# Kernel optimization log

Hardware: AMD Instinct MI355X
Metric: run time of the kernel (lower is better)

The kernel has to match this reference:

```python
import jax, jax.numpy as jnp
import numpy as np

B, T, NT, H, L, F, NH, R = 2, 1024, 30, 1024, 8, 2816, 16, 16
HD = H // NH
LORA_SCALE = 32.0 / 16.0  # lora_alpha / r
CLAMP = 10.0
EPS = 1e-6


def _rms(x, w):
    return x * jax.lax.rsqrt(jnp.mean(x * x, axis=-1, keepdims=True) + EPS) * w


def _rope(x):
    # x: [B,T,NH,HD] -- LLaMA rotary embedding
    half = HD // 2
    inv_freq = 1.0 / (10000.0 ** (jnp.arange(0, half, dtype=jnp.float32) / half))
    ang = jnp.arange(x.shape[1], dtype=jnp.float32)[:, None] * inv_freq  # [T,half]
    cos = jnp.concatenate([jnp.cos(ang), jnp.cos(ang)], -1)[None, :, None, :]
    sin = jnp.concatenate([jnp.sin(ang), jnp.sin(ang)], -1)[None, :, None, :]
    x1, x2 = x[..., :half], x[..., half:]
    return x * cos + jnp.concatenate([-x2, x1], -1) * sin


def _lora(x, W, A, Bm):
    # W: [in,out], A: [r,in], Bm: [out,r]  (dequantized base + LoRA update)
    return x @ W + ((x @ A.T) @ Bm.T) * LORA_SCALE


def setup_inputs():
    key = jax.random.key(0)
    ks = jax.random.split(key, 16)
    n = lambda k, s, sc=0.02: jax.random.normal(k, s, jnp.float32) * sc
    return {
        'x': jax.random.normal(ks[0], (B, T, NT), jnp.float32),
        'temperature': jnp.float32(1.0),
        'state_W': n(ks[1], (NT, H), 0.1),
        'state_b': jnp.zeros((H,), jnp.float32),
        'ln1': jnp.ones((L, H), jnp.float32),
        'ln2': jnp.ones((L, H), jnp.float32),
        'Wqkv': n(ks[2], (L, 3, H, H)),
        'Aqkv': n(ks[3], (L, 3, R, H)),
        'Bqkv': n(ks[4], (L, 3, H, R)),
        'Wo': n(ks[5], (L, H, H)),
        'Ao': n(ks[6], (L, R, H)),
        'Bo': n(ks[7], (L, H, R)),
        'Wgu': n(ks[8], (L, 2, H, F)),
        'Agu': n(ks[9], (L, 2, R, H)),
        'Bgu': n(ks[10], (L, 2, F, R)),
        'Wd': n(ks[11], (L, F, H)),
        'Ad': n(ks[12], (L, R, F)),
        'Bd': n(ks[13], (L, H, R)),
        'ln_f': jnp.ones((H,), jnp.float32),
        'head_W': n(ks[14], (H, NT + 1), 0.01),
        'head_b': jnp.zeros((NT + 1,), jnp.float32),
    }


def reference(x, temperature, state_W, state_b, ln1, ln2, Wqkv, Aqkv, Bqkv,
              Wo, Ao, Bo, Wgu, Agu, Bgu, Wd, Ad, Bd, ln_f, head_W, head_b):
    causal = jnp.tril(jnp.ones((T, T), bool))

    def layer(h, p):
        l1, l2, wqkv, aqkv, bqkv, wo, ao, bo, wgu, agu, bgu, wd, ad, bd = p
        hn = _rms(h, l1)
        qkv = jnp.einsum('bth,khd->kbtd', hn, wqkv)
        qkv = qkv + jnp.einsum('kbtr,kdr->kbtd',
                               jnp.einsum('bth,krh->kbtr', hn, aqkv), bqkv) * LORA_SCALE
        q = _rope(qkv[0].reshape(B, T, NH, HD))
        k = _rope(qkv[1].reshape(B, T, NH, HD))
        v = qkv[2].reshape(B, T, NH, HD)
        scores = jnp.einsum('bqhd,bkhd->bhqk', q, k) / np.sqrt(HD).astype(np.float32)
        scores = jnp.where(causal, scores, jnp.float32(-1e9))
        probs = jax.nn.softmax(scores, axis=-1)
        att = jnp.einsum('bhqk,bkhd->bqhd', probs, v).reshape(B, T, H)
        h = h + _lora(att, wo, ao, bo)
        hn2 = _rms(h, l2)
        gu = jnp.einsum('bth,khf->kbtf', hn2, wgu)
        gu = gu + jnp.einsum('kbtr,kfr->kbtf',
                             jnp.einsum('bth,krh->kbtr', hn2, agu), bgu) * LORA_SCALE
        act = jax.nn.silu(gu[0]) * gu[1]
        h = h + _lora(act, wd, ad, bd)
        return h, None

    h = x @ state_W + state_b  # state encoder -> inputs_embeds
    h, _ = jax.lax.scan(layer, h, (ln1, ln2, Wqkv, Aqkv, Bqkv, Wo, Ao, Bo,
                                   Wgu, Agu, Bgu, Wd, Ad, Bd))
    latent = _rms(h, ln_f)  # last hidden state
    logits = latent @ head_W + head_b
    logits_clamped = jnp.clip(logits, -CLAMP, CLAMP)
    portfolio_weights = jax.nn.softmax(logits_clamped / temperature, axis=-1)
    return portfolio_weights, logits_clamped
```

## Files before the change

### kernel.cpp

```cpp
#include <hip/hip_runtime.h>
#include <hip/hip_bf16.h>
#include <cstdint>

#define B_    2
#define T_    1024
#define NT_   30
#define H_    1024
#define L_    8
#define F_    2816
#define NH_   16
#define R_    16
#define HD_   64
#define M_    2048
#define NTP1_ 31

typedef unsigned short u16;
typedef short  s16x8 __attribute__((ext_vector_type(8)));
typedef unsigned short u16x4 __attribute__((ext_vector_type(4)));
typedef unsigned short u16x8 __attribute__((ext_vector_type(8)));
typedef float  f32x4 __attribute__((ext_vector_type(4)));

__device__ __forceinline__ u16 f2bf(float f){
  __hip_bfloat16 h = __float2bfloat16(f);
  return __builtin_bit_cast(unsigned short, h);
}
__device__ __forceinline__ float bf2f(u16 u){
  uint32_t v = (uint32_t)u << 16;
  return __builtin_bit_cast(float, v);
}

__device__ __forceinline__ void async16(const void* g, void* l){
  __builtin_amdgcn_global_load_lds((const __attribute__((address_space(1))) void*)g,
                                   (__attribute__((address_space(3))) void*)l, 16, 0, 0);
}

__global__ __launch_bounds__(256, 3) void fold_kernel(
    const float* __restrict__ W, const float* __restrict__ A,
    const float* __restrict__ Bm, u16* __restrict__ Wt,
    int K, int N, long strW, long strA, long strB, long strWt)
{
  const int mat = blockIdx.z;
  W  += (long)mat * strW;  A  += (long)mat * strA;
  Bm += (long)mat * strB;  Wt += (long)mat * strWt;
  const int k0 = blockIdx.x * 64, n0 = blockIdx.y * 64;
  __shared__ float Wt_s[64][65];
  __shared__ float As[16][64];
  __shared__ float Bs[64][20];
  const int tid = threadIdx.x;
  {
    const int kr = tid >> 4;
    const int n4 = (tid & 15) * 4;
    #pragma unroll
    for (int p = 0; p < 4; p++){
      int krow = p * 16 + kr;
      float4 w = *(const float4*)(W + (long)(k0 + krow) * N + n0 + n4);
      Wt_s[n4+0][krow] = w.x; Wt_s[n4+1][krow] = w.y;
      Wt_s[n4+2][krow] = w.z; Wt_s[n4+3][krow] = w.w;
    }
    const int r = tid >> 4, kc = (tid & 15) * 4;
    *(float4*)&As[r][kc] = *(const float4*)(A + (long)r * K + k0 + kc);
    const int nb = tid >> 2, r4 = (tid & 3) * 4;
    float4 b = *(const float4*)(Bm + (long)(n0 + nb) * 16 + r4);
    Bs[nb][r4+0]=b.x; Bs[nb][r4+1]=b.y; Bs[nb][r4+2]=b.z; Bs[nb][r4+3]=b.w;
  }
  __syncthreads();
  const int ko = (tid & 7) * 8;
  const int na = tid >> 3;
  float bq0[16], bq1[16];
  #pragma unroll
  for (int c = 0; c < 4; c++){
    *(float4*)&bq0[c*4] = *(const float4*)&Bs[na][c*4];
    *(float4*)&bq1[c*4] = *(const float4*)&Bs[na+32][c*4];
  }
  float l0[8] = {}, l1[8] = {};
  #pragma unroll
  for (int r = 0; r < 16; r++){
    float a[8];
    *(float4*)&a[0] = *(const float4*)&As[r][ko];
    *(float4*)&a[4] = *(const float4*)&As[r][ko+4];
    #pragma unroll
    for (int j = 0; j < 8; j++){
      l0[j] += a[j] * bq0[r];
      l1[j] += a[j] * bq1[r];
    }
  }
  u16x8 o0, o1;
  #pragma unroll
  for (int j = 0; j < 8; j++){
    o0[j] = f2bf(Wt_s[na][ko+j]    + 2.0f * l0[j]);
    o1[j] = f2bf(Wt_s[na+32][ko+j] + 2.0f * l1[j]);
  }
  *(u16x8*)(Wt + (long)(n0+na)*K    + k0 + ko) = o0;
  *(u16x8*)(Wt + (long)(n0+na+32)*K + k0 + ko) = o1;
}

__global__ __launch_bounds__(256) void embed_kernel(
    const float* __restrict__ x, const float* __restrict__ sw,
    const float* __restrict__ sb, float* __restrict__ h)
{
  const int m = blockIdx.x;
  const float* xr = x + (long)m * NT_;
  for (int jj = threadIdx.x; jj < H_; jj += 256){
    float acc = sb[jj];
    #pragma unroll
    for (int i = 0; i < NT_; i++) acc += xr[i] * sw[i * H_ + jj];
    h[(long)m * H_ + jj] = acc;
  }
}

__global__ __launch_bounds__(256) void rms_kernel(
    float* __restrict__ hsrc, const float* __restrict__ p0, const float* __restrict__ p1,
    const float* __restrict__ w, u16* __restrict__ outp, int fuse)
{
  const int m = blockIdx.x, t = threadIdx.x;
  float4 v = ((const float4*)(hsrc + (long)m * H_))[t];
  if (fuse){
    const float4 a = ((const float4*)(p0 + (long)m * H_))[t];
    const float4 b = ((const float4*)(p1 + (long)m * H_))[t];
    v.x += a.x + b.x; v.y += a.y + b.y; v.z += a.z + b.z; v.w += a.w + b.w;
    ((float4*)(hsrc + (long)m * H_))[t] = v;
  }
  float ss = v.x*v.x + v.y*v.y + v.z*v.z + v.w*v.w;
  #pragma unroll
  for (int off = 32; off >= 1; off >>= 1) ss += __shfl_xor(ss, off);
  __shared__ float red[4];
  if ((t & 63) == 0) red[t >> 6] = ss;
  __syncthreads();
  const float scale = rsqrtf((red[0]+red[1]+red[2]+red[3]) * (1.0f/H_) + 1e-6f);
  const float4 wv = ((const float4*)w)[t];
  u16x4 o;
  o[0] = f2bf(v.x*scale*wv.x); o[1] = f2bf(v.y*scale*wv.y);
  o[2] = f2bf(v.z*scale*wv.z); o[3] = f2bf(v.w*scale*wv.w);
  *(u16x4*)(outp + (long)m * H_ + t * 4) = o;
}

template<int OUTBF>
__global__ __launch_bounds__(256, 2) void gemm_bt(
    const u16* __restrict__ Ag, const u16* __restrict__ Btg, void* __restrict__ Cptr,
    int Ndim, int Klen, int Kstride, long zsA, long zsB, long zsC)
{
  Ag  += (long)blockIdx.z * zsA;
  Btg += (long)blockIdx.z * zsB;
  const int m0 = blockIdx.x * 128, n0 = blockIdx.y * 128;
  __shared__ alignas(16) u16 As[128 * 64];
  __shared__ alignas(16) u16 Bs[128 * 64];
  const int tid = threadIdx.x;
  const int wave = tid >> 6, lane = tid & 63;
  const int wm = (wave & 1) * 64, wn = (wave >> 1) * 64;
  const int fr = lane & 15, quad = lane >> 4;

  f32x4 acc[4][4] = {};

  for (int kt = 0; kt < Klen; kt += 64){
    __syncthreads();
    #pragma unroll
    for (int c = 0; c < 4; c++){
      int lin = c * 256 + tid;
      int row = lin >> 3, p = lin & 7;
      int gc = ((p ^ (row & 7)) * 8);
      async16(Ag  + (long)(m0 + row) * Kstride + kt + gc, As + lin * 8);
      async16(Btg + (long)(n0 + row) * Kstride + kt + gc, Bs + lin * 8);
    }
    __syncthreads();
    #pragma unroll
    for (int kk = 0; kk < 2; kk++){
      s16x8 af[4], bg[4];
      #pragma unroll
      for (int i = 0; i < 4; i++){
        int rA = wm + i * 16 + fr;
        af[i] = *(const s16x8*)(As + rA * 64 + (((kk*4 + quad) ^ (rA & 7)) * 8));
        int rB = wn + i * 16 + fr;
        bg[i] = *(const s16x8*)(Bs + rB * 64 + (((kk*4 + quad) ^ (rB & 7)) * 8));
      }
      #pragma unroll
      for (int i = 0; i < 4; i++)
        #pragma unroll
        for (int j = 0; j < 4; j++)
          acc[i][j] = __builtin_amdgcn_mfma_f32_16x16x32_bf16(af[i], bg[j], acc[i][j], 0, 0, 0);
    }
  }
  #pragma unroll
  for (int i = 0; i < 4; i++){
    int row0 = m0 + wm + i * 16 + quad * 4;
    #pragma unroll
    for (int j = 0; j < 4; j++){
      int col = n0 + wn + j * 16 + fr;
      #pragma unroll
      for (int r = 0; r < 4; r++){
        long idx = (long)(row0 + r) * Ndim + col;
        if (OUTBF){
          u16* C = (u16*)Cptr + (long)blockIdx.z * zsC;
          C[idx] = f2bf(acc[i][j][r]);
        } else {
          float* C = (float*)Cptr + (long)blockIdx.z * zsC;
          C[idx] = acc[i][j][r];
        }
      }
    }
  }
}

__global__ __launch_bounds__(256, 2) void gemm_gu(
    const u16* __restrict__ Ag, const u16* __restrict__ Bgw,
    const u16* __restrict__ Buw, u16* __restrict__ actb)
{
  const int m0 = blockIdx.x * 128, n0 = blockIdx.y * 128;
  __shared__ alignas(16) u16 As[128 * 64];
  __shared__ alignas(16) u16 Bg_[128 * 64];
  __shared__ alignas(16) u16 Bu_[128 * 64];
  const int tid = threadIdx.x;
  const int wave = tid >> 6, lane = tid & 63;
  const int wm = (wave & 1) * 64, wn = (wave >> 1) * 64;
  const int fr = lane & 15, quad = lane >> 4;

  f32x4 accg[4][4] = {}, accu[4][4] = {};

  for (int kt = 0; kt < H_; kt += 64){
    __syncthreads();
    #pragma unroll
    for (int c = 0; c < 4; c++){
      int lin = c * 256 + tid;
      int row = lin >> 3, p = lin & 7;
      int gc = ((p ^ (row & 7)) * 8);
      async16(Ag  + (long)(m0 + row) * H_ + kt + gc, As  + lin * 8);
      async16(Bgw + (long)(n0 + row) * H_ + kt + gc, Bg_ + lin * 8);
      async16(Buw + (long)(n0 + row) * H_ + kt + gc, Bu_ + lin * 8);
    }
    __syncthreads();
    #pragma unroll
    for (int kk = 0; kk < 2; kk++){
      s16x8 af[4], bb[4];
      #pragma unroll
      for (int i = 0; i < 4; i++){
        int rA = wm + i * 16 + fr;
        af[i] = *(const s16x8*)(As + rA * 64 + (((kk*4 + quad) ^ (rA & 7)) * 8));
      }
      #pragma unroll
      for (int i = 0; i < 4; i++){
        int rB = wn + i * 16 + fr;
        bb[i] = *(const s16x8*)(Bg_ + rB * 64 + (((kk*4 + quad) ^ (rB & 7)) * 8));
      }
      #pragma unroll
      for (int i = 0; i < 4; i++)
        #pragma unroll
        for (int j = 0; j < 4; j++)
          accg[i][j] = __builtin_amdgcn_mfma_f32_16x16x32_bf16(af[i], bb[j], accg[i][j], 0, 0, 0);
      #pragma unroll
      for (int i = 0; i < 4; i++){
        int rB = wn + i * 16 + fr;
        bb[i] = *(const s16x8*)(Bu_ + rB * 64 + (((kk*4 + quad) ^ (rB & 7)) * 8));
      }
      #pragma unroll
      for (int i = 0; i < 4; i++)
        #pragma unroll
        for (int j = 0; j < 4; j++)
          accu[i][j] = __builtin_amdgcn_mfma_f32_16x16x32_bf16(af[i], bb[j], accu[i][j], 0, 0, 0);
    }
  }
  #pragma unroll
  for (int i = 0; i < 4; i++){
    int row0 = m0 + wm + i * 16 + quad * 4;
    #pragma unroll
    for (int j = 0; j < 4; j++){
      int col = n0 + wn + j * 16 + fr;
      #pragma unroll
      for (int r = 0; r < 4; r++){
        float g = accg[i][j][r], u = accu[i][j][r];
        float act = g / (1.0f + __expf(-g)) * u;
        actb[(long)(row0 + r) * F_ + col] = f2bf(act);
      }
    }
  }
}

__global__ __launch_bounds__(256) void rope_vt_kernel(
    const u16* __restrict__ qkv, u16* __restrict__ qr, u16* __restrict__ kr,
    u16* __restrict__ vt)
{
  const int bid = blockIdx.x;
  if (bid < M_){
    const int m = bid;
    const int b = m >> 10, t = m & 1023;
    for (int w = threadIdx.x; w < 1024; w += 256){
      const int sel = w >> 9;
      const int hh  = (w >> 5) & 15;
      const int i   = w & 31;
      const u16* src = qkv + (long)m * 3072 + sel * 1024 + hh * HD_;
      float x1 = bf2f(src[i]), x2 = bf2f(src[i + 32]);
      float freq = exp2f((float)i * (-13.287712379549449f / 32.0f));
      float ang = (float)t * freq;
      float sn, cs; __sincosf(ang, &sn, &cs);
      u16* dst = (sel ? kr : qr) + ((long)((b * NH_ + hh) * T_ + t)) * HD_;
      dst[i]      = f2bf(x1 * cs - x2 * sn);
      dst[i + 32] = f2bf(x2 * cs + x1 * sn);
    }
  } else {
    const int v = bid - M_;
    const int bh = v >> 5, tch = v & 31;
    const int b = bh >> 4, hh = bh & 15;
    const int d = threadIdx.x & 63, tc = threadIdx.x >> 6;
    const int t0 = tch * 32 + tc * 8;
    const u16* src = qkv + (long)(b * T_ + t0) * 3072 + 2048 + hh * HD_ + d;
    u16x8 o;
    #pragma unroll
    for (int j = 0; j < 8; j++) o[j] = src[(long)j * 3072];
    *(u16x8*)(vt + ((long)bh * HD_ + d) * T_ + t0) = o;
  }
}

__global__ __launch_bounds__(256, 2) void attn_kernel(
    const u16* __restrict__ qr, const u16* __restrict__ kr,
    const u16* __restrict__ vt, u16* __restrict__ att)
{
  const int bh = blockIdx.y;
  const int b = bh >> 4, hh = bh & 15;
  __shared__ alignas(16) u16 Qs[64 * 64];
  __shared__ alignas(16) u16 Ks[128 * 64];
  __shared__ alignas(16) u16 Vs[64 * 128];
  __shared__ alignas(16) u16 Ps[64 * 136];
  const int tid = threadIdx.x;
  const int wave = tid >> 6, lane = tid & 63, fr = lane & 15, quad = lane >> 4;
  const int wrow = wave * 16;
  const u16* kgb = kr + (long)bh * T_ * HD_;
  const u16* vgb = vt + (long)bh * HD_ * T_;

  for (int pass = 0; pass < 2; pass++){
    const int qt = pass ? (15 - (int)blockIdx.x) : (int)blockIdx.x;
    __syncthreads();
    const u16* qg = qr + ((long)bh * T_ + qt * 64) * HD_;
    #pragma unroll
    for (int c = 0; c < 2; c++){
      int lin = c * 256 + tid, row = lin >> 3, p = lin & 7;
      async16(qg + row * HD_ + ((p ^ (row & 7)) * 8), Qs + lin * 8);
    }
    f32x4 o_acc[4] = {};
    float m_r[4] = {-1e30f, -1e30f, -1e30f, -1e30f};
    float l_r[4] = {};
    const int kmax = (qt * 64 + 63) >> 7;

    for (int kt = 0; kt <= kmax; kt++){
      __syncthreads();
      const u16* kg = kgb + (long)kt * 128 * HD_;
      #pragma unroll
      for (int c = 0; c < 4; c++){
        int lin = c * 256 + tid, row = lin >> 3, p = lin & 7;
        async16(kg + row * HD_ + ((p ^ (row & 7)) * 8), Ks + lin * 8);
      }
      #pragma unroll
      for (int c = 0; c < 4; c++){
        int lin = c * 256 + tid, row = lin >> 4, p = lin & 15;
        async16(vgb + (long)row * T_ + kt * 128 + ((p ^ (row & 15)) * 8), Vs + lin * 8);
      }
      __syncthreads();

      f32x4 s[8] = {};
      s16x8 aq[2];
      {
        int rA = wrow + fr;
        #pragma unroll
        for (int kk = 0; kk < 2; kk++)
          aq[kk] = *(const s16x8*)(Qs + rA * 64 + (((kk*4 + quad) ^ (rA & 7)) * 8));
      }
      #pragma unroll
      for (int ik = 0; ik < 8; ik++){
        #pragma unroll
        for (int kk = 0; kk < 2; kk++){
          int rB = ik * 16 + fr;
          s16x8 bk = *(const s16x8*)(Ks + rB * 64 + (((kk*4 + quad) ^ (rB & 7)) * 8));
          s[ik] = __builtin_amdgcn_mfma_f32_16x16x32_bf16(aq[kk], bk, s[ik], 0, 0, 0);
        }
      }
      const bool diag = (kt == kmax);
      #pragma unroll
      for (int r = 0; r < 4; r++){
        const int qgi = qt * 64 + wrow + quad * 4 + r;
        float tmax = -1e30f;
        #pragma unroll
        for (int ik = 0; ik < 8; ik++){
          float v = s[ik][r] * 0.125f;
          if (diag && (kt * 128 + ik * 16 + fr) > qgi) v = -1e9f;
          s[ik][r] = v;
          tmax = fmaxf(tmax, v);
        }
        #pragma unroll
        for (int off = 8; off >= 1; off >>= 1) tmax = fmaxf(tmax, __shfl_xor(tmax, off));
        const float mnew = fmaxf(m_r[r], tmax);
        const float alpha = __expf(m_r[r] - mnew);
        m_r[r] = mnew;
        float ts = 0.0f;
        const int prow = wrow + quad * 4 + r;
        #pragma unroll
        for (int ik = 0; ik < 8; ik++){
          float p = __expf(s[ik][r] - mnew);
          ts += p;
          Ps[prow * 136 + ik * 16 + fr] = f2bf(p);
        }
        #pragma unroll
        for (int off = 8; off >= 1; off >>= 1) ts += __shfl_xor(ts, off);
        l_r[r] = l_r[r] * alpha + ts;
        #pragma unroll
        for (int jd = 0; jd < 4; jd++) o_acc[jd][r] *= alpha;
      }
      #pragma unroll
      for (int kk2 = 0; kk2 < 4; kk2++){
        s16x8 ap = *(const s16x8*)(Ps + (wrow + fr) * 136 + kk2 * 32 + quad * 8);
        #pragma unroll
        for (int jd = 0; jd < 4; jd++){
          int rV = jd * 16 + fr;
          s16x8 bv = *(const s16x8*)(Vs + rV * 128 + (((kk2*4 + quad) ^ (rV & 15)) * 8));
          o_acc[jd] = __builtin_amdgcn_mfma_f32_16x16x32_bf16(ap, bv, o_acc[jd], 0, 0, 0);
        }
      }
    }
    #pragma unroll
    for (int r = 0; r < 4; r++){
      const int t_loc = qt * 64 + wrow + quad * 4 + r;
      const long rowbase = ((long)b * T_ + t_loc) * H_ + hh * HD_;
      const float inv = 1.0f / l_r[r];
      #pragma unroll
      for (int jd = 0; jd < 4; jd++)
        att[rowbase + jd * 16 + fr] = f2bf(o_acc[jd][r] * inv);
    }
  }
}

__global__ __launch_bounds__(256) void head_kernel(
    const float* __restrict__ hsrc, const float* __restrict__ p0, const float* __restrict__ p1,
    const float* __restrict__ lnf, const float* __restrict__ hw, const float* __restrict__ hb,
    const float* __restrict__ temp, float* __restrict__ outp)
{
  const int m = blockIdx.x, t = threadIdx.x;
  __shared__ float lat[H_];
  __shared__ float red[4];
  __shared__ float part[8][32];
  float4 v = ((const float4*)(hsrc + (long)m * H_))[t];
  {
    const float4 a = ((const float4*)(p0 + (long)m * H_))[t];
    const float4 b = ((const float4*)(p1 + (long)m * H_))[t];
    v.x += a.x + b.x; v.y += a.y + b.y; v.z += a.z + b.z; v.w += a.w + b.w;
  }
  float ss = v.x*v.x + v.y*v.y + v.z*v.z + v.w*v.w;
  #pragma unroll
  for (int off = 32; off >= 1; off >>= 1) ss += __shfl_xor(ss, off);
  if ((t & 63) == 0) red[t >> 6] = ss;
  __syncthreads();
  const float scale = rsqrtf((red[0]+red[1]+red[2]+red[3]) * (1.0f/H_) + 1e-6f);
  const float4 wv = ((const float4*)lnf)[t];
  lat[t*4+0] = v.x*scale*wv.x;  lat[t*4+1] = v.y*scale*wv.y;
  lat[t*4+2] = v.z*scale*wv.z;  lat[t*4+3] = v.w*scale*wv.w;
  __syncthreads();
  const int j = t & 31, seg = t >> 5;
  float pp = 0.0f;
  if (j < 31){
    const float* wp = hw + j;
    for (int k = seg * 128; k < seg * 128 + 128; k++) pp += lat[k] * wp[(long)k * 31];
  }
  part[seg][j] = pp;
  __syncthreads();
  if (t < 32){
    float dot = 0.0f;
    #pragma unroll
    for (int s2 = 0; s2 < 8; s2++) dot += part[s2][t];
    const float logit = (t < 31) ? dot + hb[t] : -1e30f;
    const float lc = fminf(fmaxf(logit, -10.0f), 10.0f);
    const float z = (t < 31) ? lc / temp[0] : -1e30f;
    float mx = z;
    #pragma unroll
    for (int off = 16; off >= 1; off >>= 1) mx = fmaxf(mx, __shfl_xor(mx, off, 32));
    const float e = (t < 31) ? __expf(z - mx) : 0.0f;
    float sum = e;
    #pragma unroll
    for (int off = 16; off >= 1; off >>= 1) sum += __shfl_xor(sum, off, 32);
    if (t < 31){
      outp[(long)m * NTP1_ + t] = e / sum;
      outp[(long)M_ * NTP1_ + (long)m * NTP1_ + t] = lc;
    }
  }
}

extern "C" void kernel_launch(void* const* d_in, const int* in_sizes, int n_in,
                              void* d_out, int out_size, void* d_ws, size_t ws_size,
                              hipStream_t stream) {
  const float* x    = (const float*)d_in[0];
  const float* temp = (const float*)d_in[1];
  const float* sW   = (const float*)d_in[2];
  const float* sb   = (const float*)d_in[3];
  const float* ln1  = (const float*)d_in[4];
  const float* ln2  = (const float*)d_in[5];
  const float* Wqkv = (const float*)d_in[6];
  const float* Aqkv = (const float*)d_in[7];
  const float* Bqkv = (const float*)d_in[8];
  const float* Wo   = (const float*)d_in[9];
  const float* Ao   = (const float*)d_in[10];
  const float* Bo   = (const float*)d_in[11];
  const float* Wgu  = (const float*)d_in[12];
  const float* Agu  = (const float*)d_in[13];
  const float* Bgu  = (const float*)d_in[14];
  const float* Wd   = (const float*)d_in[15];
  const float* Ad   = (const float*)d_in[16];
  const float* Bd   = (const float*)d_in[17];
  const float* lnf  = (const float*)d_in[18];
  const float* hW   = (const float*)d_in[19];
  const float* hb   = (const float*)d_in[20];
  float* out = (float*)d_out;

  uint8_t* ws = (uint8_t*)d_ws;
  size_t off = 0;
  auto alloc = [&](size_t bytes) -> void* {
    void* p = ws + off;
    off += (bytes + 255) & ~(size_t)255;
    return p;
  };
  u16*   wt_qkv = (u16*)  alloc((size_t)L_ * 3 * H_ * H_ * 2);
  u16*   wt_o   = (u16*)  alloc((size_t)L_ * H_ * H_ * 2);
  u16*   wt_gu  = (u16*)  alloc((size_t)L_ * 2 * F_ * H_ * 2);
  u16*   wt_d   = (u16*)  alloc((size_t)L_ * H_ * F_ * 2);
  float* h      = (float*)alloc((size_t)M_ * H_ * 4);
  u16*   hn     = (u16*)  alloc((size_t)M_ * H_ * 2);
  u16*   qkvb   = (u16*)  alloc((size_t)M_ * 3072 * 2);
  float* p0     = (float*)alloc((size_t)2 * M_ * H_ * 4);
  float* p1     = p0 + (size_t)M_ * H_;
  u16*   qr     = (u16*)  alloc((size_t)M_ * H_ * 2);
  u16*   krr    = (u16*)  alloc((size_t)M_ * H_ * 2);
  u16*   vtb    = (u16*)  alloc((size_t)M_ * H_ * 2);
  u16*   attb   = (u16*)  alloc((size_t)M_ * H_ * 2);
  u16*   actb   = (u16*)  alloc((size_t)M_ * F_ * 2);

  fold_kernel<<<dim3(16, 16, L_ * 3), 256, 0, stream>>>(Wqkv, Aqkv, Bqkv, wt_qkv,
      H_, H_, (long)H_ * H_, (long)R_ * H_, (long)H_ * R_, (long)H_ * H_);
  fold_kernel<<<dim3(16, 16, L_), 256, 0, stream>>>(Wo, Ao, Bo, wt_o,
      H_, H_, (long)H_ * H_, (long)R_ * H_, (long)H_ * R_, (long)H_ * H_);
  fold_kernel<<<dim3(16, 44, L_ * 2), 256, 0, stream>>>(Wgu, Agu, Bgu, wt_gu,
      H_, F_, (long)H_ * F_, (long)R_ * H_, (long)F_ * R_, (long)F_ * H_);
  fold_kernel<<<dim3(44, 16, L_), 256, 0, stream>>>(Wd, Ad, Bd, wt_d,
      F_, H_, (long)F_ * H_, (long)R_ * F_, (long)H_ * R_, (long)H_ * F_);

  embed_kernel<<<M_, 256, 0, stream>>>(x, sW, sb, h);

  for (int l = 0; l < L_; l++){
    rms_kernel<<<M_, 256, 0, stream>>>(h, p0, p1, ln1 + (long)l * H_, hn, l > 0 ? 1 : 0);
    gemm_bt<1><<<dim3(16, 24, 1), 256, 0, stream>>>(hn, wt_qkv + (long)l * 3 * H_ * H_,
        qkvb, 3072, 1024, 1024, 0, 0, 0);
    rope_vt_kernel<<<M_ + 1024, 256, 0, stream>>>(qkvb, qr, krr, vtb);
    attn_kernel<<<dim3(8, B_ * NH_), 256, 0, stream>>>(qr, krr, vtb, attb);
    gemm_bt<0><<<dim3(16, 8, 2), 256, 0, stream>>>(attb, wt_o + (long)l * H_ * H_,
        p0, H_, 512, H_, 512, 512, (long)M_ * H_);
    rms_kernel<<<M_, 256, 0, stream>>>(h, p0, p1, ln2 + (long)l * H_, hn, 1);
    gemm_gu<<<dim3(16, 22), 256, 0, stream>>>(hn,
        wt_gu + (long)l * 2 * F_ * H_, wt_gu + (long)l * 2 * F_ * H_ + (long)F_ * H_, actb);
    gemm_bt<0><<<dim3(16, 8, 2), 256, 0, stream>>>(actb, wt_d + (long)l * H_ * F_,
        p0, H_, 1408, F_, 1408, 1408, (long)M_ * H_);
  }

  head_kernel<<<M_, 256, 0, stream>>>(h, p0, p1, lnf, hW, hb, temp, out);
}
```

Before: 1.695 ms.

## Fuse RoPE and V-transpose into QKV GEMM epilogue; split-K 4 for down projection

The QKV GEMM now applies rotary embedding to Q/K and writes V transposed straight from its accumulators. This removes the separate rope/transpose kernel and the bf16 qkv round trip. The down-projection GEMM now splits K four ways instead of two, with a generalized split-K gemm_bt and RMS/head kernels that sum a variable number of partial buffers. This gives more blocks for occupancy at the cost of extra partial-sum traffic. Launch bounds are also raised to 3 blocks per CU.

```diff
diff --git a/kernel.cpp b/kernel.cpp
--- a/kernel.cpp
+++ b/kernel.cpp
@@ -109,15 +109,16 @@
 }
 
 __global__ __launch_bounds__(256) void rms_kernel(
-    float* __restrict__ hsrc, const float* __restrict__ p0, const float* __restrict__ p1,
-    const float* __restrict__ w, u16* __restrict__ outp, int fuse)
+    float* __restrict__ hsrc, const float* __restrict__ pb,
+    const float* __restrict__ w, u16* __restrict__ outp, int nparts)
 {
   const int m = blockIdx.x, t = threadIdx.x;
   float4 v = ((const float4*)(hsrc + (long)m * H_))[t];
-  if (fuse){
-    const float4 a = ((const float4*)(p0 + (long)m * H_))[t];
-    const float4 b = ((const float4*)(p1 + (long)m * H_))[t];
-    v.x += a.x + b.x; v.y += a.y + b.y; v.z += a.z + b.z; v.w += a.w + b.w;
+  if (nparts){
+    for (int k = 0; k < nparts; k++){
+      const float4 a = ((const float4*)(pb + (long)k * M_ * H_ + (long)m * H_))[t];
+      v.x += a.x; v.y += a.y; v.z += a.z; v.w += a.w;
+    }
     ((float4*)(hsrc + (long)m * H_))[t] = v;
   }
   float ss = v.x*v.x + v.y*v.y + v.z*v.z + v.w*v.w;
@@ -135,12 +136,16 @@
 }
 
 template<int OUTBF>
-__global__ __launch_bounds__(256, 2) void gemm_bt(
+__global__ __launch_bounds__(256, 3) void gemm_bt(
     const u16* __restrict__ Ag, const u16* __restrict__ Btg, void* __restrict__ Cptr,
-    int Ndim, int Klen, int Kstride, long zsA, long zsB, long zsC)
-{
-  Ag  += (long)blockIdx.z * zsA;
-  Btg += (long)blockIdx.z * zsB;
+    int Ndim, int Kstride, int Ksteps, long zsC)
+{
+  const int z = blockIdx.z, Z = (int)gridDim.z;
+  const int kb = Ksteps / Z, rem = Ksteps % Z;
+  const int sblk = (z < rem) ? z * (kb + 1) : rem * (kb + 1) + (z - rem) * kb;
+  const int klen = (kb + (z < rem ? 1 : 0)) * 64;
+  Ag  += (long)sblk * 64;
+  Btg += (long)sblk * 64;
   const int m0 = blockIdx.x * 128, n0 = blockIdx.y * 128;
   __shared__ alignas(16) u16 As[128 * 64];
   __shared__ alignas(16) u16 Bs[128 * 64];
@@ -151,7 +156,7 @@
 
   f32x4 acc[4][4] = {};
 
-  for (int kt = 0; kt < Klen; kt += 64){
+  for (int kt = 0; kt < klen; kt += 64){
     __syncthreads();
     #pragma unroll
     for (int c = 0; c < 4; c++){
@@ -200,6 +205,89 @@
   }
 }
 
+__global__ __launch_bounds__(256, 3) void gemm_qkv(
+    const u16* __restrict__ Ag, const u16* __restrict__ Btg,
+    u16* __restrict__ qr, u16* __restrict__ kr, u16* __restrict__ vt)
+{
+  const int m0 = blockIdx.x * 128, n0 = blockIdx.y * 128;
+  __shared__ alignas(16) u16 As[128 * 64];
+  __shared__ alignas(16) u16 Bs[128 * 64];
+  const int tid = threadIdx.x;
+  const int wave = tid >> 6, lane = tid & 63;
+  const int wm = (wave & 1) * 64, wn = (wave >> 1) * 64;
+  const int fr = lane & 15, quad = lane >> 4;
+
+  f32x4 acc[4][4] = {};
+
+  for (int kt = 0; kt < H_; kt += 64){
+    __syncthreads();
+    #pragma unroll
+    for (int c = 0; c < 4; c++){
+      int lin = c * 256 + tid;
+      int row = lin >> 3, p = lin & 7;
+      int gc = ((p ^ (row & 7)) * 8);
+      async16(Ag  + (long)(m0 + row) * H_ + kt + gc, As + lin * 8);
+      async16(Btg + (long)(n0 + row) * H_ + kt + gc, Bs + lin * 8);
+    }
+    __syncthreads();
+    #pragma unroll
+    for (int kk = 0; kk < 2; kk++){
+      s16x8 af[4], bg[4];
+      #pragma unroll
+      for (int i = 0; i < 4; i++){
+        int rA = wm + i * 16 + fr;
+        af[i] = *(const s16x8*)(As + rA * 64 + (((kk*4 + quad) ^ (rA & 7)) * 8));
+        int rB = wn + i * 16 + fr;
+        bg[i] = *(const s16x8*)(Bs + rB * 64 + (((kk*4 + quad) ^ (rB & 7)) * 8));
+      }
+      #pragma unroll
+      for (int i = 0; i < 4; i++)
+        #pragma unroll
+        for (int j = 0; j < 4; j++)
+          acc[i][j] = __builtin_amdgcn_mfma_f32_16x16x32_bf16(af[i], bg[j], acc[i][j], 0, 0, 0);
+    }
+  }
+  const int sel  = n0 >> 10;
+  const int nloc = (n0 & 1023) + wn;
+  const int hh   = nloc >> 6;
+  if (sel == 2){
+    #pragma unroll
+    for (int i = 0; i < 4; i++){
+      int row0 = m0 + wm + i * 16 + quad * 4;
+      int b = row0 >> 10, t0 = row0 & 1023;
+      #pragma unroll
+      for (int j = 0; j < 4; j++){
+        int d = j * 16 + fr;
+        u16x4 o;
+        #pragma unroll
+        for (int r = 0; r < 4; r++) o[r] = f2bf(acc[i][j][r]);
+        *(u16x4*)(vt + ((long)((b * NH_ + hh) * HD_ + d)) * T_ + t0) = o;
+      }
+    }
+  } else {
+    u16* dst = sel ? kr : qr;
+    #pragma unroll
+    for (int i = 0; i < 4; i++){
+      int row0 = m0 + wm + i * 16 + quad * 4;
+      int b = row0 >> 10;
+      #pragma unroll
+      for (int j = 0; j < 2; j++){
+        int d1 = j * 16 + fr;
+        float freq = exp2f((float)d1 * (-13.287712379549449f / 32.0f));
+        #pragma unroll
+        for (int r = 0; r < 4; r++){
+          int t = (row0 + r) & 1023;
+          float x1 = acc[i][j][r], x2 = acc[i][j + 2][r];
+          float sn, cs; __sincosf((float)t * freq, &sn, &cs);
+          long base = ((long)(b * NH_ + hh) * T_ + t) * HD_;
+          dst[base + d1]      = f2bf(x1 * cs - x2 * sn);
+          dst[base + d1 + 32] = f2bf(x2 * cs + x1 * sn);
+        }
+      }
+    }
+  }
+}
+
 __global__ __launch_bounds__(256, 2) void gemm_gu(
     const u16* __restrict__ Ag, const u16* __restrict__ Bgw,
     const u16* __restrict__ Buw, u16* __restrict__ actb)
@@ -270,41 +358,6 @@
         actb[(long)(row0 + r) * F_ + col] = f2bf(act);
       }
     }
-  }
-}
-
-__global__ __launch_bounds__(256) void rope_vt_kernel(
-    const u16* __restrict__ qkv, u16* __restrict__ qr, u16* __restrict__ kr,
-    u16* __restrict__ vt)
-{
-  const int bid = blockIdx.x;
-  if (bid < M_){
-    const int m = bid;
-    const int b = m >> 10, t = m & 1023;
-    for (int w = threadIdx.x; w < 1024; w += 256){
-      const int sel = w >> 9;
-      const int hh  = (w >> 5) & 15;
-      const int i   = w & 31;
-      const u16* src = qkv + (long)m * 3072 + sel * 1024 + hh * HD_;
-      float x1 = bf2f(src[i]), x2 = bf2f(src[i + 32]);
-      float freq = exp2f((float)i * (-13.287712379549449f / 32.0f));
-      float ang = (float)t * freq;
-      float sn, cs; __sincosf(ang, &sn, &cs);
-      u16* dst = (sel ? kr : qr) + ((long)((b * NH_ + hh) * T_ + t)) * HD_;
-      dst[i]      = f2bf(x1 * cs - x2 * sn);
-      dst[i + 32] = f2bf(x2 * cs + x1 * sn);
-    }
-  } else {
-    const int v = bid - M_;
-    const int bh = v >> 5, tch = v & 31;
-    const int b = bh >> 4, hh = bh & 15;
-    const int d = threadIdx.x & 63, tc = threadIdx.x >> 6;
-    const int t0 = tch * 32 + tc * 8;
-    const u16* src = qkv + (long)(b * T_ + t0) * 3072 + 2048 + hh * HD_ + d;
-    u16x8 o;
-    #pragma unroll
-    for (int j = 0; j < 8; j++) o[j] = src[(long)j * 3072];
-    *(u16x8*)(vt + ((long)bh * HD_ + d) * T_ + t0) = o;
   }
 }
 
@@ -425,7 +478,7 @@
 }
 
 __global__ __launch_bounds__(256) void head_kernel(
-    const float* __restrict__ hsrc, const float* __restrict__ p0, const float* __restrict__ p1,
+    const float* __restrict__ hsrc, const float* __restrict__ pb,
     const float* __restrict__ lnf, const float* __restrict__ hw, const float* __restrict__ hb,
     const float* __restrict__ temp, float* __restrict__ outp)
 {
@@ -434,10 +487,10 @@
   __shared__ float red[4];
   __shared__ float part[8][32];
   float4 v = ((const float4*)(hsrc + (long)m * H_))[t];
-  {
-    const float4 a = ((const float4*)(p0 + (long)m * H_))[t];
-    const float4 b = ((const float4*)(p1 + (long)m * H_))[t];
-    v.x += a.x + b.x; v.y += a.y + b.y; v.z += a.z + b.z; v.w += a.w + b.w;
+  #pragma unroll
+  for (int k = 0; k < 4; k++){
+    const float4 a = ((const float4*)(pb + (long)k * M_ * H_ + (long)m * H_))[t];
+    v.x += a.x; v.y += a.y; v.z += a.z; v.w += a.w;
   }
   float ss = v.x*v.x + v.y*v.y + v.z*v.z + v.w*v.w;
   #pragma unroll
@@ -517,9 +570,7 @@
   u16*   wt_d   = (u16*)  alloc((size_t)L_ * H_ * F_ * 2);
   float* h      = (float*)alloc((size_t)M_ * H_ * 4);
   u16*   hn     = (u16*)  alloc((size_t)M_ * H_ * 2);
-  u16*   qkvb   = (u16*)  alloc((size_t)M_ * 3072 * 2);
-  float* p0     = (float*)alloc((size_t)2 * M_ * H_ * 4);
-  float* p1     = p0 + (size_t)M_ * H_;
+  float* p0     = (float*)alloc((size_t)4 * M_ * H_ * 4);
   u16*   qr     = (u16*)  alloc((size_t)M_ * H_ * 2);
   u16*   krr    = (u16*)  alloc((size_t)M_ * H_ * 2);
   u16*   vtb    = (u16*)  alloc((size_t)M_ * H_ * 2);
@@ -538,19 +589,18 @@
   embed_kernel<<<M_, 256, 0, stream>>>(x, sW, sb, h);
 
   for (int l = 0; l < L_; l++){
-    rms_kernel<<<M_, 256, 0, stream>>>(h, p0, p1, ln1 + (long)l * H_, hn, l > 0 ? 1 : 0);
-    gemm_bt<1><<<dim3(16, 24, 1), 256, 0, stream>>>(hn, wt_qkv + (long)l * 3 * H_ * H_,
-        qkvb, 3072, 1024, 1024, 0, 0, 0);
-    rope_vt_kernel<<<M_ + 1024, 256, 0, stream>>>(qkvb, qr, krr, vtb);
+    rms_kernel<<<M_, 256, 0, stream>>>(h, p0, ln1 + (long)l * H_, hn, l > 0 ? 4 : 0);
+    gemm_qkv<<<dim3(16, 24), 256, 0, stream>>>(hn, wt_qkv + (long)l * 3 * H_ * H_,
+        qr, krr, vtb);
     attn_kernel<<<dim3(8, B_ * NH_), 256, 0, stream>>>(qr, krr, vtb, attb);
     gemm_bt<0><<<dim3(16, 8, 2), 256, 0, stream>>>(attb, wt_o + (long)l * H_ * H_,
-        p0, H_, 512, H_, 512, 512, (long)M_ * H_);
-    rms_kernel<<<M_, 256, 0, stream>>>(h, p0, p1, ln2 + (long)l * H_, hn, 1);
+        p0, H_, H_, 16, (long)M_ * H_);
+    rms_kernel<<<M_, 256, 0, stream>>>(h, p0, ln2 + (long)l * H_, hn, 2);
     gemm_gu<<<dim3(16, 22), 256, 0, stream>>>(hn,
         wt_gu + (long)l * 2 * F_ * H_, wt_gu + (long)l * 2 * F_ * H_ + (long)F_ * H_, actb);
-    gemm_bt<0><<<dim3(16, 8, 2), 256, 0, stream>>>(actb, wt_d + (long)l * H_ * F_,
-        p0, H_, 1408, F_, 1408, 1408, (long)M_ * H_);
-  }
-
-  head_kernel<<<M_, 256, 0, stream>>>(h, p0, p1, lnf, hW, hb, temp, out);
-}
+    gemm_bt<0><<<dim3(16, 8, 4), 256, 0, stream>>>(actb, wt_d + (long)l * H_ * F_,
+        p0, H_, F_, 44, (long)M_ * H_);
+  }
+
+  head_kernel<<<M_, 256, 0, stream>>>(h, p0, lnf, hW, hb, temp, out);
+}
```

New measurement: 1.590 ms. 6.2% less time.
